# Optimization experiments

Hardware: AMD Instinct MI355X
Metric: run time of the kernel (lower is better)

The kernel has to match this reference:

```python
import jax, jax.numpy as jnp
import numpy as np

N, E, D = 10000, 160000, 512


def setup_inputs() -> dict:
    key = jax.random.key(0)
    ks = jax.random.split(key, 5)
    x = jax.random.normal(ks[0], (N, D), dtype=jnp.float32)
    edge_index = jax.random.randint(ks[1], (2, E), 0, N, dtype=jnp.int32)
    W = jax.random.normal(ks[2], (D, D), dtype=jnp.float32) * (1.0 / np.sqrt(D))
    a_src = jax.random.normal(ks[3], (D,), dtype=jnp.float32) * 0.1
    a_dst = jax.random.normal(ks[4], (D,), dtype=jnp.float32) * 0.1
    bias = jnp.zeros((D,), dtype=jnp.float32)
    return {"x": x, "edge_index": edge_index, "W": W,
            "a_src": a_src, "a_dst": a_dst, "bias": bias}


def reference(x, edge_index, W, a_src, a_dst, bias):
    n = x.shape[0]
    # PyG GATConv default: add self-loops
    loops = jnp.arange(n, dtype=edge_index.dtype)
    src = jnp.concatenate([edge_index[0], loops])  # [E+N]
    dst = jnp.concatenate([edge_index[1], loops])  # [E+N]

    h = x @ W.T                                    # [N, D] linear projection
    e_src = h @ a_src                              # [N]
    e_dst = h @ a_dst                              # [N]
    e = e_src[src] + e_dst[dst]                    # [E+N]
    neg_slope = 0.2
    e = jnp.where(e > 0, e, neg_slope * e)         # leaky_relu

    # per-destination softmax (stable); self-loops guarantee non-empty segments
    m = jax.ops.segment_max(e, dst, num_segments=n)
    e = jnp.exp(e - m[dst])
    s = jax.ops.segment_sum(e, dst, num_segments=n)
    alpha = e / s[dst]                             # [E+N]

    msg = alpha[:, None] * h[src]                  # [E+N, D]
    out = jax.ops.segment_sum(msg, dst, num_segments=n) + bias  # [N, D]

    # module forward: x + elu(gat(x, edge_index))
    return x + jax.nn.elu(out)
```

## Files before the change

kernel.cpp:

```cpp
#include <hip/hip_runtime.h>
#include <hip/hip_bf16.h>

using bf16x8 = __attribute__((ext_vector_type(8))) __bf16;
using f32x4  = __attribute__((ext_vector_type(4))) float;
typedef unsigned int u32;

#define DFEAT 512
#define SLOTS 64

static __device__ __forceinline__ unsigned short f2bfbits(float f) {
    union { float f; unsigned int u; } v; v.f = f;
    unsigned int u = v.u;
    unsigned int r = (u + 0x7fffu + ((u >> 16) & 1u)) >> 16;
    return (unsigned short)r;
}

static __device__ __forceinline__ void gload16(const unsigned short* g, unsigned short* l) {
    __builtin_amdgcn_global_load_lds(
        (const __attribute__((address_space(1))) u32*)g,
        (__attribute__((address_space(3))) u32*)l, 16, 0, 0);
}

__global__ __launch_bounds__(256) void cvt_scatter_kernel(
    const float* __restrict__ x, const float* __restrict__ w,
    unsigned short* __restrict__ Xb, unsigned short* __restrict__ Wb,
    const int* __restrict__ srcv, const int* __restrict__ dstv,
    int* __restrict__ cur, int* __restrict__ slot,
    int nx4, int ntot4, int E, int T)
{
    int i = blockIdx.x * 256 + threadIdx.x;
    if (i < ntot4) {
        const float* in = (i < nx4) ? x : w;
        unsigned short* o = (i < nx4) ? Xb : Wb;
        int j = (i < nx4) ? i : i - nx4;
        float4 v = ((const float4*)in)[j];
        ushort4 u;
        u.x = f2bfbits(v.x); u.y = f2bfbits(v.y);
        u.z = f2bfbits(v.z); u.w = f2bfbits(v.w);
        ((ushort4*)o)[j] = u;
    }
    if (i < T) {
        int s, d;
        if (i < E) { s = srcv[i]; d = dstv[i]; }
        else       { s = d = i - E; }
        int pos = atomicAdd(&cur[d], 1);
        if (pos < SLOTS) slot[(size_t)d * SLOTS + pos] = s;
    }
}

__global__ __launch_bounds__(256, 3) void gemm_h_kernel(
    const unsigned short* __restrict__ X, const unsigned short* __restrict__ Wm,
    const float* __restrict__ avs, const float* __restrict__ avd,
    unsigned short* __restrict__ H, float* __restrict__ es, float* __restrict__ ed,
    int N)
{
    __shared__ __align__(16) unsigned short Asm[2][128 * 64];
    __shared__ __align__(16) unsigned short Bsm[2][64 * 64];

    int L = blockIdx.x;
    int xcd = L & 7;
    int q   = L >> 3;
    int rpan = (q >> 3) * 8 + xcd;
    int cpan = q & 7;
    int rowPanels = (N + 127) >> 7;
    if (rpan >= rowPanels) return;
    int bm = rpan * 128;
    int bn = cpan * 64;

    int tid  = threadIdx.x;
    int wave = tid >> 6;
    int lane = tid & 63;
    int l15  = lane & 15;
    int quad = lane >> 4;

    int srow   = lane >> 3;
    int schunk = (lane & 7) ^ srow;
    const unsigned short* gA0;
    const unsigned short* gA1;
    const unsigned short* gA2;
    const unsigned short* gA3;
    {
        int r0 = bm + wave * 32 +  0 + srow; r0 = r0 < N ? r0 : N - 1;
        int r1 = bm + wave * 32 +  8 + srow; r1 = r1 < N ? r1 : N - 1;
        int r2 = bm + wave * 32 + 16 + srow; r2 = r2 < N ? r2 : N - 1;
        int r3 = bm + wave * 32 + 24 + srow; r3 = r3 < N ? r3 : N - 1;
        gA0 = X + (size_t)r0 * DFEAT + schunk * 8;
        gA1 = X + (size_t)r1 * DFEAT + schunk * 8;
        gA2 = X + (size_t)r2 * DFEAT + schunk * 8;
        gA3 = X + (size_t)r3 * DFEAT + schunk * 8;
    }
    const unsigned short* gB0 = Wm + (size_t)(bn + wave * 16 + srow) * DFEAT + schunk * 8;
    const unsigned short* gB1 = gB0 + (size_t)8 * DFEAT;

    auto stage = [&](int buf, int s) {
        int ko = s * 64;
        gload16(gA0 + ko, &Asm[buf][(wave * 32 +  0) * 64]);
        gload16(gA1 + ko, &Asm[buf][(wave * 32 +  8) * 64]);
        gload16(gA2 + ko, &Asm[buf][(wave * 32 + 16) * 64]);
        gload16(gA3 + ko, &Asm[buf][(wave * 32 + 24) * 64]);
        gload16(gB0 + ko, &Bsm[buf][(wave * 16 + 0) * 64]);
        gload16(gB1 + ko, &Bsm[buf][(wave * 16 + 8) * 64]);
    };

    f32x4 acc[2][4] = {};
    int xa = l15 & 7;
    int aoff0 = (wave * 32 +  0 + l15) * 128;
    int aoff1 = (wave * 32 + 16 + l15) * 128;

    auto compute = [&](int buf) {
        const char* Ab = (const char*)&Asm[buf][0];
        const char* Bb = (const char*)&Bsm[buf][0];
        #pragma unroll
        for (int ks = 0; ks < 2; ++ks) {
            int cb = ((ks * 4 + quad) ^ xa) * 16;
            bf16x8 a0 = *(const bf16x8*)(Ab + aoff0 + cb);
            bf16x8 a1 = *(const bf16x8*)(Ab + aoff1 + cb);
            bf16x8 b0 = *(const bf16x8*)(Bb + (0 * 16 + l15) * 128 + cb);
            bf16x8 b1 = *(const bf16x8*)(Bb + (1 * 16 + l15) * 128 + cb);
            bf16x8 b2 = *(const bf16x8*)(Bb + (2 * 16 + l15) * 128 + cb);
            bf16x8 b3 = *(const bf16x8*)(Bb + (3 * 16 + l15) * 128 + cb);
            acc[0][0] = __builtin_amdgcn_mfma_f32_16x16x32_bf16(a0, b0, acc[0][0], 0, 0, 0);
            acc[1][0] = __builtin_amdgcn_mfma_f32_16x16x32_bf16(a1, b0, acc[1][0], 0, 0, 0);
            acc[0][1] = __builtin_amdgcn_mfma_f32_16x16x32_bf16(a0, b1, acc[0][1], 0, 0, 0);
            acc[1][1] = __builtin_amdgcn_mfma_f32_16x16x32_bf16(a1, b1, acc[1][1], 0, 0, 0);
            acc[0][2] = __builtin_amdgcn_mfma_f32_16x16x32_bf16(a0, b2, acc[0][2], 0, 0, 0);
            acc[1][2] = __builtin_amdgcn_mfma_f32_16x16x32_bf16(a1, b2, acc[1][2], 0, 0, 0);
            acc[0][3] = __builtin_amdgcn_mfma_f32_16x16x32_bf16(a0, b3, acc[0][3], 0, 0, 0);
            acc[1][3] = __builtin_amdgcn_mfma_f32_16x16x32_bf16(a1, b3, acc[1][3], 0, 0, 0);
        }
    };

    stage(0, 0);
    __syncthreads();
    int buf = 0;
    for (int s = 0; s < 7; ++s) {
        stage(buf ^ 1, s + 1);
        compute(buf);
        __syncthreads();
        buf ^= 1;
    }
    compute(buf);

    float as[4], ad[4];
    #pragma unroll
    for (int nt = 0; nt < 4; ++nt) {
        as[nt] = avs[bn + nt * 16 + l15];
        ad[nt] = avd[bn + nt * 16 + l15];
    }

    #pragma unroll
    for (int mt = 0; mt < 2; ++mt) {
        int rbase = bm + wave * 32 + mt * 16 + quad * 4;
        #pragma unroll
        for (int nt = 0; nt < 4; ++nt) {
            int col = bn + nt * 16 + l15;
            #pragma unroll
            for (int r = 0; r < 4; ++r) {
                int row = rbase + r;
                if (row < N) H[(size_t)row * DFEAT + col] = f2bfbits(acc[mt][nt][r]);
            }
        }
        #pragma unroll
        for (int r = 0; r < 4; ++r) {
            float ps = acc[mt][0][r] * as[0] + acc[mt][1][r] * as[1]
                     + acc[mt][2][r] * as[2] + acc[mt][3][r] * as[3];
            float pd = acc[mt][0][r] * ad[0] + acc[mt][1][r] * ad[1]
                     + acc[mt][2][r] * ad[2] + acc[mt][3][r] * ad[3];
            #pragma unroll
            for (int m = 1; m < 16; m <<= 1) {
                ps += __shfl_xor(ps, m);
                pd += __shfl_xor(pd, m);
            }
            int row = rbase + r;
            if (l15 == 0 && row < N) {
                atomicAdd(&es[row], ps);
                atomicAdd(&ed[row], pd);
            }
        }
    }
}

__global__ __launch_bounds__(256) void aggregate_kernel(
    const unsigned short* __restrict__ H, const float* __restrict__ x,
    const float* __restrict__ bias,
    const int* __restrict__ cur, const int* __restrict__ slot,
    const float* __restrict__ es, const float* __restrict__ ed,
    float* __restrict__ out, int N)
{
    int node = (blockIdx.x * 256 + threadIdx.x) >> 6;
    int lane = threadIdx.x & 63;
    if (node >= N) return;

    int k = cur[node];
    if (k > SLOTS) k = SLOTS;

    int   s = 0;
    float w = 0.f;
    if (lane < k) {
        s = slot[(size_t)node * SLOTS + lane];
        float e = es[s] + ed[node];
        e = e > 0.f ? e : 0.2f * e;
        w = __expf(e);
    }
    float denom = w;
    #pragma unroll
    for (int off = 32; off > 0; off >>= 1) denom += __shfl_xor(denom, off);
    float inv = 1.0f / denom;

    float a[8] = {};
    const unsigned short* Hl = H + lane * 8;

    auto fma8 = [&](uint4 hv, float wj) {
        a[0] += wj * __uint_as_float(hv.x << 16);
        a[1] += wj * __uint_as_float(hv.x & 0xffff0000u);
        a[2] += wj * __uint_as_float(hv.y << 16);
        a[3] += wj * __uint_as_float(hv.y & 0xffff0000u);
        a[4] += wj * __uint_as_float(hv.z << 16);
        a[5] += wj * __uint_as_float(hv.z & 0xffff0000u);
        a[6] += wj * __uint_as_float(hv.w << 16);
        a[7] += wj * __uint_as_float(hv.w & 0xffff0000u);
    };

    int j = 0;
    for (; j + 7 < k; j += 8) {
        int   s0 = __shfl(s, j),     s1 = __shfl(s, j + 1);
        int   s2 = __shfl(s, j + 2), s3 = __shfl(s, j + 3);
        int   s4 = __shfl(s, j + 4), s5 = __shfl(s, j + 5);
        int   s6 = __shfl(s, j + 6), s7 = __shfl(s, j + 7);
        float w0 = __shfl(w, j),     w1 = __shfl(w, j + 1);
        float w2 = __shfl(w, j + 2), w3 = __shfl(w, j + 3);
        float w4 = __shfl(w, j + 4), w5 = __shfl(w, j + 5);
        float w6 = __shfl(w, j + 6), w7 = __shfl(w, j + 7);
        uint4 h0 = *(const uint4*)(Hl + (size_t)s0 * DFEAT);
        uint4 h1 = *(const uint4*)(Hl + (size_t)s1 * DFEAT);
        uint4 h2 = *(const uint4*)(Hl + (size_t)s2 * DFEAT);
        uint4 h3 = *(const uint4*)(Hl + (size_t)s3 * DFEAT);
        uint4 h4 = *(const uint4*)(Hl + (size_t)s4 * DFEAT);
        uint4 h5 = *(const uint4*)(Hl + (size_t)s5 * DFEAT);
        uint4 h6 = *(const uint4*)(Hl + (size_t)s6 * DFEAT);
        uint4 h7 = *(const uint4*)(Hl + (size_t)s7 * DFEAT);
        fma8(h0, w0); fma8(h1, w1); fma8(h2, w2); fma8(h3, w3);
        fma8(h4, w4); fma8(h5, w5); fma8(h6, w6); fma8(h7, w7);
    }
    if (j + 3 < k) {
        int   s0 = __shfl(s, j),     s1 = __shfl(s, j + 1);
        int   s2 = __shfl(s, j + 2), s3 = __shfl(s, j + 3);
        float w0 = __shfl(w, j),     w1 = __shfl(w, j + 1);
        float w2 = __shfl(w, j + 2), w3 = __shfl(w, j + 3);
        uint4 h0 = *(const uint4*)(Hl + (size_t)s0 * DFEAT);
        uint4 h1 = *(const uint4*)(Hl + (size_t)s1 * DFEAT);
        uint4 h2 = *(const uint4*)(Hl + (size_t)s2 * DFEAT);
        uint4 h3 = *(const uint4*)(Hl + (size_t)s3 * DFEAT);
        fma8(h0, w0); fma8(h1, w1); fma8(h2, w2); fma8(h3, w3);
        j += 4;
    }
    for (; j < k; ++j) {
        uint4 hv = *(const uint4*)(Hl + (size_t)__shfl(s, j) * DFEAT);
        fma8(hv, __shfl(w, j));
    }

    int c = lane * 8;
    float4 b0 = *(const float4*)(bias + c);
    float4 b1 = *(const float4*)(bias + c + 4);
    float4 x0 = *(const float4*)(x + (size_t)node * DFEAT + c);
    float4 x1 = *(const float4*)(x + (size_t)node * DFEAT + c + 4);
    float r[8];
    r[0] = a[0] * inv + b0.x; r[1] = a[1] * inv + b0.y;
    r[2] = a[2] * inv + b0.z; r[3] = a[3] * inv + b0.w;
    r[4] = a[4] * inv + b1.x; r[5] = a[5] * inv + b1.y;
    r[6] = a[6] * inv + b1.z; r[7] = a[7] * inv + b1.w;
    #pragma unroll
    for (int i = 0; i < 8; ++i)
        r[i] = r[i] > 0.f ? r[i] : __expf(r[i]) - 1.f;
    float4 o0 = make_float4(x0.x + r[0], x0.y + r[1], x0.z + r[2], x0.w + r[3]);
    float4 o1 = make_float4(x1.x + r[4], x1.y + r[5], x1.z + r[6], x1.w + r[7]);
    *(float4*)(out + (size_t)node * DFEAT + c)     = o0;
    *(float4*)(out + (size_t)node * DFEAT + c + 4) = o1;
}

extern "C" void kernel_launch(void* const* d_in, const int* in_sizes, int n_in,
                              void* d_out, int out_size, void* d_ws, size_t ws_size,
                              hipStream_t stream)
{
    const float* x    = (const float*)d_in[0];
    const int*   edge = (const int*)d_in[1];
    const float* Wm   = (const float*)d_in[2];
    const float* avs  = (const float*)d_in[3];
    const float* avd  = (const float*)d_in[4];
    const float* bias = (const float*)d_in[5];

    const int D = DFEAT;
    const int N = in_sizes[0] / D;
    const int E = in_sizes[1] / 2;
    const int T = E + N;
    const int* srcv = edge;
    const int* dstv = edge + E;

    char* ws = (char*)d_ws;
    size_t off = 0;
    auto alloc = [&](size_t bytes) -> char* {
        char* p = ws + off;
        off += (bytes + 255) & ~(size_t)255;
        return p;
    };
    int*   cur  = (int*)alloc((size_t)N * 3 * 4);
    float* es   = (float*)(cur + N);
    float* ed   = es + N;
    int*   slot = (int*)alloc((size_t)N * SLOTS * 4);
    unsigned short* Xb = (unsigned short*)alloc((size_t)N * D * 2);
    unsigned short* Wb = (unsigned short*)alloc((size_t)D * D * 2);
    unsigned short* H  = (unsigned short*)alloc((size_t)N * D * 2);

    hipMemsetAsync(cur, 0, (size_t)N * 3 * 4, stream);

    int nx4   = (N * D) / 4;
    int ntot4 = nx4 + (D * D) / 4;
    int grid0 = (ntot4 > T ? ntot4 : T);
    cvt_scatter_kernel<<<dim3((grid0 + 255) / 256), 256, 0, stream>>>(
        x, Wm, Xb, Wb, srcv, dstv, cur, slot, nx4, ntot4, E, T);

    int rowPanels  = (N + 127) / 128;
    int rowPanels8 = ((rowPanels + 7) / 8) * 8;
    gemm_h_kernel<<<dim3(rowPanels8 * 8), 256, 0, stream>>>(
        Xb, Wb, avs, avd, H, es, ed, N);
    aggregate_kernel<<<dim3((N * 64 + 255) / 256), 256, 0, stream>>>(
        H, x, bias, cur, slot, es, ed, (float*)d_out, N);
}
```

Measured before the change: 132.9 us.

## Fuse fp32-to-bf16 conversion of x into GEMM A-tile loading

```diff
diff --git a/kernel.cpp b/kernel.cpp
--- a/kernel.cpp
+++ b/kernel.cpp
@@ -15,29 +15,32 @@
     return (unsigned short)r;
 }
 
+static __device__ __forceinline__ bf16x8 cvt8(float4 u, float4 v) {
+    bf16x8 r;
+    r[0] = (__bf16)u.x; r[1] = (__bf16)u.y; r[2] = (__bf16)u.z; r[3] = (__bf16)u.w;
+    r[4] = (__bf16)v.x; r[5] = (__bf16)v.y; r[6] = (__bf16)v.z; r[7] = (__bf16)v.w;
+    return r;
+}
+
 static __device__ __forceinline__ void gload16(const unsigned short* g, unsigned short* l) {
     __builtin_amdgcn_global_load_lds(
         (const __attribute__((address_space(1))) u32*)g,
         (__attribute__((address_space(3))) u32*)l, 16, 0, 0);
 }
 
-__global__ __launch_bounds__(256) void cvt_scatter_kernel(
-    const float* __restrict__ x, const float* __restrict__ w,
-    unsigned short* __restrict__ Xb, unsigned short* __restrict__ Wb,
+__global__ __launch_bounds__(256) void prep_kernel(
+    const float* __restrict__ w, unsigned short* __restrict__ Wb,
     const int* __restrict__ srcv, const int* __restrict__ dstv,
     int* __restrict__ cur, int* __restrict__ slot,
-    int nx4, int ntot4, int E, int T)
+    int nw4, int E, int T)
 {
     int i = blockIdx.x * 256 + threadIdx.x;
-    if (i < ntot4) {
-        const float* in = (i < nx4) ? x : w;
-        unsigned short* o = (i < nx4) ? Xb : Wb;
-        int j = (i < nx4) ? i : i - nx4;
-        float4 v = ((const float4*)in)[j];
+    if (i < nw4) {
+        float4 v = ((const float4*)w)[i];
         ushort4 u;
         u.x = f2bfbits(v.x); u.y = f2bfbits(v.y);
         u.z = f2bfbits(v.z); u.w = f2bfbits(v.w);
-        ((ushort4*)o)[j] = u;
+        ((ushort4*)Wb)[i] = u;
     }
     if (i < T) {
         int s, d;
@@ -49,7 +52,7 @@
 }
 
 __global__ __launch_bounds__(256, 3) void gemm_h_kernel(
-    const unsigned short* __restrict__ X, const unsigned short* __restrict__ Wm,
+    const float* __restrict__ Xf, const unsigned short* __restrict__ Wm,
     const float* __restrict__ avs, const float* __restrict__ avd,
     unsigned short* __restrict__ H, float* __restrict__ es, float* __restrict__ ed,
     int N)
@@ -75,31 +78,41 @@
 
     int srow   = lane >> 3;
     int schunk = (lane & 7) ^ srow;
-    const unsigned short* gA0;
-    const unsigned short* gA1;
-    const unsigned short* gA2;
-    const unsigned short* gA3;
-    {
-        int r0 = bm + wave * 32 +  0 + srow; r0 = r0 < N ? r0 : N - 1;
-        int r1 = bm + wave * 32 +  8 + srow; r1 = r1 < N ? r1 : N - 1;
-        int r2 = bm + wave * 32 + 16 + srow; r2 = r2 < N ? r2 : N - 1;
-        int r3 = bm + wave * 32 + 24 + srow; r3 = r3 < N ? r3 : N - 1;
-        gA0 = X + (size_t)r0 * DFEAT + schunk * 8;
-        gA1 = X + (size_t)r1 * DFEAT + schunk * 8;
-        gA2 = X + (size_t)r2 * DFEAT + schunk * 8;
-        gA3 = X + (size_t)r3 * DFEAT + schunk * 8;
-    }
     const unsigned short* gB0 = Wm + (size_t)(bn + wave * 16 + srow) * DFEAT + schunk * 8;
     const unsigned short* gB1 = gB0 + (size_t)8 * DFEAT;
 
-    auto stage = [&](int buf, int s) {
+    auto stageB = [&](int buf, int s) {
         int ko = s * 64;
-        gload16(gA0 + ko, &Asm[buf][(wave * 32 +  0) * 64]);
-        gload16(gA1 + ko, &Asm[buf][(wave * 32 +  8) * 64]);
-        gload16(gA2 + ko, &Asm[buf][(wave * 32 + 16) * 64]);
-        gload16(gA3 + ko, &Asm[buf][(wave * 32 + 24) * 64]);
         gload16(gB0 + ko, &Bsm[buf][(wave * 16 + 0) * 64]);
         gload16(gB1 + ko, &Bsm[buf][(wave * 16 + 8) * 64]);
+    };
+
+    int arl   = lane >> 1;
+    int ac0   = (lane & 1) * 4;
+    int arow  = bm + wave * 32 + arl;
+    arow = arow < N ? arow : N - 1;
+    const float* gA = Xf + (size_t)arow * DFEAT + ac0 * 8;
+    int ldsrow = wave * 32 + arl;
+    char* AbW0 = (char*)&Asm[0][0] + ldsrow * 128;
+    char* AbW1 = (char*)&Asm[1][0] + ldsrow * 128;
+    int axor = arl & 7;
+
+    float4 av[8];
+    auto aload = [&](int s) {
+        const float* p = gA + s * 64;
+        #pragma unroll
+        for (int i = 0; i < 4; ++i) {
+            av[2 * i]     = *(const float4*)(p + i * 8);
+            av[2 * i + 1] = *(const float4*)(p + i * 8 + 4);
+        }
+    };
+    auto awrite = [&](int buf) {
+        char* Ab = buf ? AbW1 : AbW0;
+        #pragma unroll
+        for (int i = 0; i < 4; ++i) {
+            bf16x8 o = cvt8(av[2 * i], av[2 * i + 1]);
+            *(bf16x8*)(Ab + (((ac0 + i) ^ axor) * 16)) = o;
+        }
     };
 
     f32x4 acc[2][4] = {};
@@ -130,12 +143,16 @@
         }
     };
 
-    stage(0, 0);
+    stageB(0, 0);
+    aload(0);
+    awrite(0);
     __syncthreads();
     int buf = 0;
     for (int s = 0; s < 7; ++s) {
-        stage(buf ^ 1, s + 1);
+        stageB(buf ^ 1, s + 1);
+        aload(s + 1);
         compute(buf);
+        awrite(buf ^ 1);
         __syncthreads();
         buf ^= 1;
     }
@@ -307,22 +324,20 @@
     float* es   = (float*)(cur + N);
     float* ed   = es + N;
     int*   slot = (int*)alloc((size_t)N * SLOTS * 4);
-    unsigned short* Xb = (unsigned short*)alloc((size_t)N * D * 2);
     unsigned short* Wb = (unsigned short*)alloc((size_t)D * D * 2);
     unsigned short* H  = (unsigned short*)alloc((size_t)N * D * 2);
 
     hipMemsetAsync(cur, 0, (size_t)N * 3 * 4, stream);
 
-    int nx4   = (N * D) / 4;
-    int ntot4 = nx4 + (D * D) / 4;
-    int grid0 = (ntot4 > T ? ntot4 : T);
-    cvt_scatter_kernel<<<dim3((grid0 + 255) / 256), 256, 0, stream>>>(
-        x, Wm, Xb, Wb, srcv, dstv, cur, slot, nx4, ntot4, E, T);
+    int nw4   = (D * D) / 4;
+    int grid0 = (nw4 > T ? nw4 : T);
+    prep_kernel<<<dim3((grid0 + 255) / 256), 256, 0, stream>>>(
+        Wm, Wb, srcv, dstv, cur, slot, nw4, E, T);
 
     int rowPanels  = (N + 127) / 128;
     int rowPanels8 = ((rowPanels + 7) / 8) * 8;
     gemm_h_kernel<<<dim3(rowPanels8 * 8), 256, 0, stream>>>(
-        Xb, Wb, avs, avd, H, es, ed, N);
+        x, Wb, avs, avd, H, es, ed, N);
     aggregate_kernel<<<dim3((N * 64 + 255) / 256), 256, 0, stream>>>(
         H, x, bias, cur, slot, es, ed, (float*)d_out, N);
 }
```

Result: slower. 148.0 us (+11.4%).
